# Kernel optimization log

Hardware: AMD Instinct MI355X
Metric: run time of the kernel (lower is better)

Reference implementation:

```python
import jax, jax.numpy as jnp
import numpy as np

B, T, D = 2, 2048, 1024
H, DK, DV, NH = 8, 128, 256, 2  # heads, key dim, value dim (expand_v=2), num_householder
CONV = 4
INTER = 2816
EPS = 1e-6


def rmsnorm(x, w):
    return x * jax.lax.rsqrt(jnp.mean(x * x, -1, keepdims=True) + EPS) * w


def l2norm(x):
    return x * jax.lax.rsqrt(jnp.sum(x * x, -1, keepdims=True) + 1e-6)


def causal_conv_silu(x, w):
    # depthwise causal conv1d with silu activation; x: [B,T,C], w: [C,K]
    K = w.shape[1]
    xp = jnp.pad(x, ((0, 0), (K - 1, 0), (0, 0)))
    y = sum(xp[:, i:i + x.shape[1], :] * w[:, i] for i in range(K))
    return jax.nn.silu(y)


def setup_inputs():
    key = jax.random.key(0)
    ks = jax.random.split(key, 16)
    s = 0.02
    return {
        "hidden_states": jax.random.normal(ks[0], (B, T, D), jnp.float32),
        "attn_norm_w": jnp.ones((D,), jnp.float32),
        "Wq": jax.random.normal(ks[1], (D, H * DK), jnp.float32) * s,
        "Wk": jax.random.normal(ks[2], (D, NH * H * DK), jnp.float32) * s,
        "Wv": jax.random.normal(ks[3], (D, NH * H * DV), jnp.float32) * s,
        "Wb": jax.random.normal(ks[4], (D, H * NH), jnp.float32) * s,
        "Wa": jax.random.normal(ks[5], (D, H), jnp.float32) * s,
        "A_log": jnp.log(jax.random.uniform(ks[6], (H,), jnp.float32, 1.0, 16.0)),
        "dt_bias": jax.random.normal(ks[7], (H,), jnp.float32) * 0.5,
        "conv_q_w": jax.random.normal(ks[8], (H * DK, CONV), jnp.float32) * 0.5,
        "conv_k_w": jax.random.normal(ks[9], (NH * H * DK, CONV), jnp.float32) * 0.5,
        "conv_v_w": jax.random.normal(ks[10], (NH * H * DV, CONV), jnp.float32) * 0.5,
        "Wg": jax.random.normal(ks[11], (D, H * DV), jnp.float32) * s,
        "o_norm_w": jnp.ones((DV,), jnp.float32),
        "Wo": jax.random.normal(ks[12], (H * DV, D), jnp.float32) * s,
        "mlp_norm_w": jnp.ones((D,), jnp.float32),
        "Wgate": jax.random.normal(ks[13], (D, 2 * INTER), jnp.float32) * s,
        "Wdown": jax.random.normal(ks[14], (INTER, D), jnp.float32) * s,
    }


def reference(hidden_states, attn_norm_w, Wq, Wk, Wv, Wb, Wa, A_log, dt_bias,
              conv_q_w, conv_k_w, conv_v_w, Wg, o_norm_w, Wo,
              mlp_norm_w, Wgate, Wdown):
    residual = hidden_states
    x = rmsnorm(hidden_states, attn_norm_w)

    # projections + short conv + silu, then L2-normalized q/k (gated delta rule)
    q = l2norm(causal_conv_silu(x @ Wq, conv_q_w).reshape(B, T, H, DK))
    k = l2norm(causal_conv_silu(x @ Wk, conv_k_w).reshape(B, T, NH, H, DK))
    v = causal_conv_silu(x @ Wv, conv_v_w).reshape(B, T, NH, H, DV)
    beta = jax.nn.sigmoid(x @ Wb).reshape(B, T, H, NH)
    g = -jnp.exp(A_log) * jax.nn.softplus(x @ Wa + dt_bias)  # [B,T,H] log-decay

    def step(S, inp):
        q_t, k_t, v_t, b_t, g_t = inp
        # forget gate applied once per token, then NH Householder delta-rule updates
        S = S * jnp.exp(g_t)[..., None, None]  # S: [B,H,DK,DV]
        for j in range(NH):
            kj, vj, bj = k_t[:, j], v_t[:, j], b_t[..., j]
            kS = jnp.einsum('bhk,bhkv->bhv', kj, S)
            S = S + bj[..., None, None] * jnp.einsum('bhk,bhv->bhkv', kj, vj - kS)
        o_t = jnp.einsum('bhk,bhkv->bhv', q_t, S)
        return S, o_t

    S0 = jnp.zeros((B, H, DK, DV), x.dtype)
    xs = (jnp.swapaxes(q, 0, 1), jnp.swapaxes(k, 0, 1), jnp.swapaxes(v, 0, 1),
          jnp.swapaxes(beta, 0, 1), jnp.swapaxes(g, 0, 1))
    _, o = jax.lax.scan(step, S0, xs)  # [T,B,H,DV]
    o = jnp.swapaxes(o, 0, 1)

    # gated RMSNorm output gate + output projection
    gate = (x @ Wg).reshape(B, T, H, DV)
    o = rmsnorm(o, o_norm_w) * jax.nn.silu(gate)
    hidden = residual + o.reshape(B, T, H * DV) @ Wo

    # GatedMLP (swiglu)
    y = rmsnorm(hidden, mlp_norm_w)
    gate_m, up = jnp.split(y @ Wgate, 2, -1)
    return hidden + (jax.nn.silu(gate_m) * up) @ Wdown
```

## Files before the change

kernel.cpp:

```cpp
#include <hip/hip_runtime.h>
#include <hip/hip_bf16.h>
#include <math.h>

#define Bq 2
#define Tq 2048
#define Dq 1024
#define Hq 8
#define DKq 128
#define DVq 256
#define NHq 2
#define BTq (Bq*Tq)
#define INTERq 2816

typedef __hip_bfloat16 bf16;
typedef short bfv8 __attribute__((ext_vector_type(8)));
typedef float f32v4 __attribute__((ext_vector_type(4)));

__device__ __forceinline__ float b2f(bf16 v){ return __bfloat162float(v); }
__device__ __forceinline__ bf16 f2b(float v){ return __float2bfloat16(v); }
__device__ __forceinline__ float bs2f(short s){
  union { short s; bf16 b; } u; u.s = s; return __bfloat162float(u.b);
}

__device__ __forceinline__ int is_f32(const unsigned* magic){ return magic[0] == 0x3F800000u; }

__device__ __forceinline__ float ldin(const void* p, int f32, size_t i){
  return f32 ? ((const float*)p)[i] : b2f(((const bf16*)p)[i]);
}

__device__ __forceinline__ void gload_lds16(const bf16* g, bf16* lds_uniform){
  __builtin_amdgcn_global_load_lds(
      (const __attribute__((address_space(1))) void*)g,
      (__attribute__((address_space(3))) void*)lds_uniform, 16, 0, 0);
}

__device__ __forceinline__ float wave_sum(float v){
  #pragma unroll
  for (int off = 32; off > 0; off >>= 1) v += __shfl_xor(v, off, 64);
  return v;
}

__device__ __forceinline__ float block_reduce_sum(float v, float* red){
  #pragma unroll
  for (int off = 32; off > 0; off >>= 1) v += __shfl_down(v, off, 64);
  int lane = threadIdx.x & 63, wid = threadIdx.x >> 6;
  if (lane == 0) red[wid] = v;
  __syncthreads();
  int nw = (blockDim.x + 63) >> 6;
  float tot = 0.f;
  for (int i = 0; i < nw; i++) tot += red[i];
  return tot;
}

struct WSplitArgs {
  const void* W[7];
  bf16* hi[7];
  bf16* lo[7];
  int K[7];
  int N[7];
  int il[7];
  int cum[8];
};

__global__ __launch_bounds__(256) void wsplit_all_kernel(WSplitArgs a,
    const unsigned* __restrict__ magic){
  __shared__ float tile[32][33];
  int f32 = is_f32(magic);
  int bid = blockIdx.x;
  int wi = 0;
  #pragma unroll
  for (int i = 1; i < 7; i++) if (bid >= a.cum[i]) wi = i;
  int rem = bid - a.cum[wi];
  const void* W = a.W[wi];
  bf16* hi = a.hi[wi];
  bf16* lo = a.lo[wi];
  int K = a.K[wi], N = a.N[wi], il = a.il[wi];
  int nbx = N >> 5;
  int n0 = (rem % nbx) * 32, k0 = (rem / nbx) * 32;
  int tx = threadIdx.x & 31, ty = threadIdx.x >> 5;
  #pragma unroll
  for (int r = 0; r < 4; r++){
    int kr = ty + r*8;
    tile[kr][tx] = ldin(W, f32, (size_t)(k0 + kr)*N + n0 + tx);
  }
  __syncthreads();
  int NH2 = N >> 1;
  #pragma unroll
  for (int r = 0; r < 4; r++){
    int nl = ty + r*8;
    int nr = n0 + nl;
    float v = tile[tx][nl];
    bf16 h = f2b(v);
    int cp = nr;
    if (il) cp = (nr < NH2) ? (((nr >> 4) << 5) | (nr & 15))
                            : ((((nr - NH2) >> 4) << 5) | 16 | ((nr - NH2) & 15));
    size_t idx = (size_t)cp*K + k0 + tx;
    hi[idx] = h;
    if (f32) lo[idx] = f2b(v - b2f(h));
  }
}

__device__ __forceinline__ void gemm_acc_bf16(const bf16* __restrict__ A,
    const bf16* __restrict__ Bh, int K, size_t bm, size_t bn,
    bf16* As, bf16* Bs, f32v4 (&acc)[4][4]){
  int tid = threadIdx.x;
  int lane = tid & 63, w = tid >> 6;
  int wm = w >> 1, wn = w & 1;
  int l15 = lane & 15, quad = lane >> 4;
  int srow = tid >> 2;
  int scol = (tid & 3) * 8;
  const bf16* Ag = A  + (bm + srow)*(size_t)K + scol;
  const bf16* Bg = Bh + (bn + srow)*(size_t)K + scol;
  int wslot = w * 512;
  int ntiles = K >> 5;
  int aoff = (wm*64 + l15)*32 + quad*8;
  int boff = (wn*64 + l15)*32 + quad*8;

#define STAGE(buf, kt) { \
    const bf16* a0 = Ag + ((size_t)(kt) << 5); \
    const bf16* b0 = Bg + ((size_t)(kt) << 5); \
    gload_lds16(a0,                &As[(buf)*4096 + wslot]); \
    gload_lds16(a0 + 64*(size_t)K, &As[(buf)*4096 + 2048 + wslot]); \
    gload_lds16(b0,                &Bs[(buf)*4096 + wslot]); \
    gload_lds16(b0 + 64*(size_t)K, &Bs[(buf)*4096 + 2048 + wslot]); }

  STAGE(0, 0)
  if (ntiles > 1) STAGE(1, 1)
  for (int t = 0; t < ntiles; ++t){
    if (t + 1 < ntiles) asm volatile("s_waitcnt vmcnt(4)" ::: "memory");
    else                asm volatile("s_waitcnt vmcnt(0)" ::: "memory");
    __builtin_amdgcn_sched_barrier(0);
    __builtin_amdgcn_s_barrier();
    __builtin_amdgcn_sched_barrier(0);
    int cur = t % 3;
    if (t + 2 < ntiles) STAGE((t + 2) % 3, t + 2)
    bfv8 a[4], bb[4];
    #pragma unroll
    for (int mt = 0; mt < 4; mt++)
      a[mt] = *(const bfv8*)(&As[cur*4096 + aoff + mt*16*32]);
    #pragma unroll
    for (int nn = 0; nn < 4; nn++)
      bb[nn] = *(const bfv8*)(&Bs[cur*4096 + boff + nn*16*32]);
    #pragma unroll
    for (int nn = 0; nn < 4; nn++)
      #pragma unroll
      for (int mt = 0; mt < 4; mt++)
        acc[mt][nn] = __builtin_amdgcn_mfma_f32_16x16x32_bf16(a[mt], bb[nn], acc[mt][nn], 0, 0, 0);
  }
#undef STAGE
}

__device__ __forceinline__ void gemm_acc_f32(const bf16* __restrict__ A,
    const bf16* __restrict__ Bh0, const bf16* __restrict__ Bl0,
    int K, size_t bm, size_t bn, f32v4 (&acc)[4][4]){
  int tid = threadIdx.x;
  int lane = tid & 63, w = tid >> 6;
  int wm = w >> 1, wn = w & 1;
  int l15 = lane & 15, quad = lane >> 4;
  const bf16* Ab = A   + (bm + wm*64 + l15)*(size_t)K + quad*8;
  const bf16* Bh = Bh0 + (bn + wn*64 + l15)*(size_t)K + quad*8;
  const bf16* Bl = Bl0 + (bn + wn*64 + l15)*(size_t)K + quad*8;
  for (int k0 = 0; k0 < K; k0 += 32){
    bfv8 a[4];
    #pragma unroll
    for (int mt = 0; mt < 4; mt++)
      a[mt] = *(const bfv8*)(Ab + (size_t)mt*16*K + k0);
    #pragma unroll
    for (int nt = 0; nt < 4; nt++){
      bfv8 bh = *(const bfv8*)(Bh + (size_t)nt*16*K + k0);
      bfv8 bl = *(const bfv8*)(Bl + (size_t)nt*16*K + k0);
      #pragma unroll
      for (int mt = 0; mt < 4; mt++){
        acc[mt][nt] = __builtin_amdgcn_mfma_f32_16x16x32_bf16(a[mt], bh, acc[mt][nt], 0, 0, 0);
        acc[mt][nt] = __builtin_amdgcn_mfma_f32_16x16x32_bf16(a[mt], bl, acc[mt][nt], 0, 0, 0);
      }
    }
  }
}

__global__ __launch_bounds__(256) void gemm_mfma_kernel(
    const bf16* __restrict__ A, const bf16* __restrict__ WThi, const bf16* __restrict__ WTlo,
    const unsigned* __restrict__ magic,
    const void* __restrict__ res, int res_mode,
    void* __restrict__ out, int out_mode,
    int M, int N, int K){
  __shared__ bf16 As[3*128*32];
  __shared__ bf16 Bs[3*128*32];
  int f32 = is_f32(magic);
  int tid = threadIdx.x;
  int lane = tid & 63, w = tid >> 6;
  int wm = w >> 1, wn = w & 1;
  int l15 = lane & 15, quad = lane >> 4;
  size_t bm = (size_t)blockIdx.x * 128, bn = (size_t)blockIdx.y * 128;

  f32v4 acc[4][4];
  #pragma unroll
  for (int mt = 0; mt < 4; mt++)
    #pragma unroll
    for (int nt = 0; nt < 4; nt++) acc[mt][nt] = 0.f;

  if (f32) gemm_acc_f32(A, WThi, WTlo, K, bm, bn, acc);
  else     gemm_acc_bf16(A, WThi, K, bm, bn, As, Bs, acc);

  if (out_mode == 3){
    #pragma unroll
    for (int mt = 0; mt < 4; mt++)
      #pragma unroll
      for (int nt = 0; nt < 4; nt += 2)
        #pragma unroll
        for (int r = 0; r < 4; r++){
          size_t row = bm + wm*64 + mt*16 + quad*4 + r;
          size_t col = (bn >> 1) + wn*32 + (nt >> 1)*16 + l15;
          float g = acc[mt][nt][r], u = acc[mt][nt+1][r];
          ((bf16*)out)[row*INTERq + col] = f2b(g / (1.f + __expf(-g)) * u);
        }
    return;
  }
  #pragma unroll
  for (int mt = 0; mt < 4; mt++)
    #pragma unroll
    for (int nt = 0; nt < 4; nt++)
      #pragma unroll
      for (int r = 0; r < 4; r++){
        size_t row = bm + wm*64 + mt*16 + quad*4 + r;
        size_t col = bn + wn*64 + nt*16 + l15;
        float v = acc[mt][nt][r];
        if (res_mode == 1) v += ldin(res, f32, row*N + col);
        else if (res_mode == 2) v += ((const float*)res)[row*N + col];
        if (out_mode == 0) ((float*)out)[row*N + col] = v;
        else if (out_mode == 1) ((bf16*)out)[row*N + col] = f2b(v);
        else { if (f32) ((float*)out)[row*N + col] = v; else ((bf16*)out)[row*N + col] = f2b(v); }
      }
}

struct QkvgArgs {
  const bf16* bh[4];
  const bf16* bl[4];
  bf16* out[4];
  int N[4];
  int yoff[5];
};

__global__ __launch_bounds__(256) void gemm_qkvg_kernel(
    const bf16* __restrict__ A, QkvgArgs a, const unsigned* __restrict__ magic){
  __shared__ bf16 As[3*128*32];
  __shared__ bf16 Bs[3*128*32];
  int f32 = is_f32(magic);
  int y = blockIdx.y;
  int g = 0;
  #pragma unroll
  for (int i = 1; i < 4; i++) if (y >= a.yoff[i]) g = i;
  size_t bm = (size_t)blockIdx.x * 128;
  size_t bn = (size_t)(y - a.yoff[g]) * 128;
  int N = a.N[g];

  f32v4 acc[4][4];
  #pragma unroll
  for (int mt = 0; mt < 4; mt++)
    #pragma unroll
    for (int nt = 0; nt < 4; nt++) acc[mt][nt] = 0.f;

  if (f32) gemm_acc_f32(A, a.bh[g], a.bl[g], 1024, bm, bn, acc);
  else     gemm_acc_bf16(A, a.bh[g], 1024, bm, bn, As, Bs, acc);

  bf16* out = a.out[g];
  int tid = threadIdx.x;
  int lane = tid & 63, w = tid >> 6;
  int wm = w >> 1, wn = w & 1;
  int l15 = lane & 15, quad = lane >> 4;
  #pragma unroll
  for (int mt = 0; mt < 4; mt++)
    #pragma unroll
    for (int nt = 0; nt < 4; nt++)
      #pragma unroll
      for (int r = 0; r < 4; r++){
        size_t row = bm + wm*64 + mt*16 + quad*4 + r;
        size_t col = bn + wn*64 + nt*16 + l15;
        out[row*N + col] = f2b(acc[mt][nt][r]);
      }
}

__global__ __launch_bounds__(256) void rmsnorm_betag_kernel(
    const void* __restrict__ hs, const void* __restrict__ attn_nw,
    const void* __restrict__ Wb, const void* __restrict__ Wa,
    const void* __restrict__ A_log, const void* __restrict__ dt_bias,
    const unsigned* __restrict__ magic,
    bf16* __restrict__ xout, float* __restrict__ beta, float* __restrict__ eg){
  __shared__ float xs[Dq];
  __shared__ float red[4];
  int f32 = is_f32(magic);
  size_t bt = blockIdx.x;
  int i0 = threadIdx.x * 4;
  float xv[4];
  if (f32){
    float4 v = *(const float4*)((const float*)hs + bt*Dq + i0);
    xv[0]=v.x; xv[1]=v.y; xv[2]=v.z; xv[3]=v.w;
  } else {
    short4 s = *(const short4*)((const bf16*)hs + bt*Dq + i0);
    xv[0]=bs2f(s.x); xv[1]=bs2f(s.y); xv[2]=bs2f(s.z); xv[3]=bs2f(s.w);
  }
  float ss = fmaf(xv[0],xv[0], fmaf(xv[1],xv[1], fmaf(xv[2],xv[2], xv[3]*xv[3])));
  float tot = block_reduce_sum(ss, red);
  float sc = rsqrtf(tot / (float)Dq + 1e-6f);
  bf16 ob[4];
  #pragma unroll
  for (int j = 0; j < 4; j++){
    float xn = xv[j] * sc * ldin(attn_nw, f32, i0 + j);
    ob[j] = f2b(xn);
    xs[i0 + j] = xn;
  }
  *(short4*)(xout + bt*Dq + i0) = *(short4*)ob;
  __syncthreads();

  int wv = threadIdx.x >> 6, lane = threadIdx.x & 63;
  #pragma unroll
  for (int r = 0; r < 6; r++){
    int n = wv*6 + r;
    float a = 0.f;
    if (n < 16){
      #pragma unroll
      for (int e = 0; e < 16; e++){
        int i = lane + 64*e;
        a = fmaf(xs[i], ldin(Wb, f32, (size_t)i*16 + n), a);
      }
    } else {
      int h = n - 16;
      #pragma unroll
      for (int e = 0; e < 16; e++){
        int i = lane + 64*e;
        a = fmaf(xs[i], ldin(Wa, f32, (size_t)i*8 + h), a);
      }
    }
    #pragma unroll
    for (int off = 32; off > 0; off >>= 1) a += __shfl_down(a, off, 64);
    if (lane == 0){
      if (n < 16){
        int h = n >> 1, j = n & 1;
        beta[(bt*Hq + h)*NHq + j] = 1.f / (1.f + expf(-a));
      } else {
        int h = n - 16;
        a += ldin(dt_bias, f32, h);
        float sp = (a > 20.f) ? a : log1pf(expf(a));
        eg[bt*Hq + h] = expf(-expf(ldin(A_log, f32, h)) * sp);
      }
    }
  }
}

__global__ __launch_bounds__(256) void rmsnorm_kernel(const void* __restrict__ in, int in_mode,
    const void* __restrict__ w, const unsigned* __restrict__ magic,
    bf16* __restrict__ out){
  __shared__ float red[4];
  int f32 = is_f32(magic);
  int inf32 = in_mode ? 1 : f32;
  size_t row = blockIdx.x;
  int i0 = threadIdx.x * 4;
  float xv[4];
  if (inf32){
    float4 v = *(const float4*)((const float*)in + row*Dq + i0);
    xv[0]=v.x; xv[1]=v.y; xv[2]=v.z; xv[3]=v.w;
  } else {
    short4 s = *(const short4*)((const bf16*)in + row*Dq + i0);
    xv[0]=bs2f(s.x); xv[1]=bs2f(s.y); xv[2]=bs2f(s.z); xv[3]=bs2f(s.w);
  }
  float ss = fmaf(xv[0],xv[0], fmaf(xv[1],xv[1], fmaf(xv[2],xv[2], xv[3]*xv[3])));
  float tot = block_reduce_sum(ss, red);
  float sc = rsqrtf(tot / (float)Dq + 1e-6f);
  bf16 ob[4];
  #pragma unroll
  for (int j = 0; j < 4; j++) ob[j] = f2b(xv[j] * sc * ldin(w, f32, i0 + j));
  *(short4*)(out + row*Dq + i0) = *(short4*)ob;
}

__global__ __launch_bounds__(64) void conv_qk_kernel(
    const bf16* __restrict__ qpre, const bf16* __restrict__ kpre,
    const void* __restrict__ wq, const void* __restrict__ wk,
    const unsigned* __restrict__ magic,
    float* __restrict__ qn, float* __restrict__ kn){
  int f32 = is_f32(magic);
  int bt = blockIdx.x;
  int t = bt & (Tq - 1);
  int yb = blockIdx.y;
  const bf16* in; const void* w; int C, cb; float* outf;
  if (yb < 8){ in = qpre; w = wq; C = 1024; cb = yb;     outf = qn; }
  else       { in = kpre; w = wk; C = 2048; cb = yb - 8; outf = kn; }
  int c = cb*128 + threadIdx.x*2;
  float a0 = 0.f, a1 = 0.f;
  #pragma unroll
  for (int i = 0; i < 4; i++){
    int tt = t - 3 + i;
    if (tt >= 0){
      short2 s = *(const short2*)(in + (size_t)(bt - 3 + i)*C + c);
      a0 = fmaf(bs2f(s.x), ldin(w, f32, (size_t)c*4 + i), a0);
      a1 = fmaf(bs2f(s.y), ldin(w, f32, (size_t)(c+1)*4 + i), a1);
    }
  }
  float y0 = a0 / (1.f + __expf(-a0));
  float y1 = a1 / (1.f + __expf(-a1));
  float tot = wave_sum(fmaf(y0, y0, y1*y1));
  float sc = rsqrtf(tot + 1e-6f);
  *(float2*)(outf + (size_t)bt*C + c) = make_float2(y0*sc, y1*sc);
}

__global__ __launch_bounds__(256) void conv_v_kernel(
    const bf16* __restrict__ in, const void* __restrict__ w,
    const unsigned* __restrict__ magic, bf16* __restrict__ out){
  int f32 = is_f32(magic);
  int bt = blockIdx.x;
  int t = bt & (Tq - 1);
  int c = blockIdx.y * 2048 + threadIdx.x * 8;
  float wv[32];
  #pragma unroll
  for (int j = 0; j < 8; j++)
    #pragma unroll
    for (int i = 0; i < 4; i++) wv[j*4+i] = ldin(w, f32, (size_t)(c+j)*4 + i);
  float acc[8] = {0,0,0,0,0,0,0,0};
  #pragma unroll
  for (int i = 0; i < 4; i++){
    int tt = t - 3 + i;
    if (tt >= 0){
      bfv8 v = *(const bfv8*)(in + (size_t)(bt - 3 + i)*4096 + c);
      #pragma unroll
      for (int j = 0; j < 8; j++) acc[j] = fmaf(bs2f(v[j]), wv[j*4+i], acc[j]);
    }
  }
  bf16 ob[8];
  #pragma unroll
  for (int j = 0; j < 8; j++) ob[j] = f2b(acc[j] / (1.f + __expf(-acc[j])));
  *(bfv8*)(out + (size_t)bt*4096 + c) = *(bfv8*)ob;
}

#define DPP_ADD(x, ctrl) ((x) + __int_as_float(__builtin_amdgcn_update_dpp( \
    0, __float_as_int(x), (ctrl), 0xF, 0xF, true)))
#define KRED(p) { p = DPP_ADD(p, 0x128); p = DPP_ADD(p, 0x124); \
                  p = DPP_ADD(p, 0x122); p = DPP_ADD(p, 0x121); }

__global__ __launch_bounds__(64, 1) void scan_kernel(
    const float* __restrict__ qn,
    const float* __restrict__ kn,
    const bf16*  __restrict__ vcv,
    const float* __restrict__ beta,
    const float* __restrict__ eg,
    float* __restrict__ o){
  int bh = blockIdx.x;
  int b = bh >> 3, h = bh & 7;
  int lane = threadIdx.x;
  int kg = lane & 15;
  int vloc = lane >> 4;
  int vv = blockIdx.y * 4 + vloc;
  int c0 = (h << 8) + vv;
  int c1 = 2048 + (h << 8) + vv;
  const size_t base = (size_t)b * Tq;
  const float* knh = kn + base*2048 + h*DKq + kg*8;
  const float* qnh = qn + (base*Hq + h)*(size_t)DKq + kg*8;
  const bf16*  vph = vcv + base*4096;
  const float* gh  = eg + base*Hq + h;
  const float2* bph = (const float2*)(beta + (base*Hq + h)*(size_t)NHq);
  float* oh = o + (base*Hq + h)*(size_t)DVq + vv;

  float4 S0 = {0,0,0,0}, S1 = {0,0,0,0};
#define SDOT(Ka, Kb, p) { \
    float e0 = fmaf(Ka.x, S0.x, Ka.y * S0.y); \
    float e1 = fmaf(Ka.z, S0.z, Ka.w * S0.w); \
    float e2 = fmaf(Kb.x, S1.x, Kb.y * S1.y); \
    float e3 = fmaf(Kb.z, S1.z, Kb.w * S1.w); \
    p = (e0 + e1) + (e2 + e3); }
#define SUPD(Ka, Kb, d) { \
    S0.x = fmaf(Ka.x, d, S0.x); S0.y = fmaf(Ka.y, d, S0.y); \
    S0.z = fmaf(Ka.z, d, S0.z); S0.w = fmaf(Ka.w, d, S0.w); \
    S1.x = fmaf(Kb.x, d, S1.x); S1.y = fmaf(Kb.y, d, S1.y); \
    S1.z = fmaf(Kb.z, d, S1.z); S1.w = fmaf(Kb.w, d, S1.w); }

  float4 A0E = *(const float4*)(knh);
  float4 A1E = *(const float4*)(knh + 4);
  float4 B0E = *(const float4*)(knh + 1024);
  float4 B1E = *(const float4*)(knh + 1028);
  float4 Q0E = *(const float4*)(qnh);
  float4 Q1E = *(const float4*)(qnh + 4);
  float4 A0O = *(const float4*)(knh + 2048);
  float4 A1O = *(const float4*)(knh + 2052);
  float4 B0O = *(const float4*)(knh + 3072);
  float4 B1O = *(const float4*)(knh + 3076);
  float4 Q0O = *(const float4*)(qnh + 1024);
  float4 Q1O = *(const float4*)(qnh + 1028);
  float  gE  = gh[0],   gO  = gh[8];
  float2 beE = bph[0],  beO = bph[8];
  float vaE = b2f(vph[c0]),        vbE = b2f(vph[c1]);
  float vaO = b2f(vph[4096 + c0]), vbO = b2f(vph[4096 + c1]);

#define STEP(A0,A1,B0,B1,Q0,Q1, gS, beS, vaS, vbS, t, tp) { \
    float egv = gS; \
    gS = gh[(tp)*8]; \
    S0.x *= egv; S0.y *= egv; S0.z *= egv; S0.w *= egv; \
    S1.x *= egv; S1.y *= egv; S1.z *= egv; S1.w *= egv; \
     \
    { float p; SDOT(A0, A1, p) \
      KRED(p) \
      float delta = beS.x * (vaS - p); \
      SUPD(A0, A1, delta) \
      A0 = *(const float4*)(knh + (tp)*2048); \
      A1 = *(const float4*)(knh + (tp)*2048 + 4); \
      vaS = b2f(vph[(tp)*4096 + c0]); } \
     \
    { float p; SDOT(B0, B1, p) \
      KRED(p) \
      float delta = beS.y * (vbS - p); \
      SUPD(B0, B1, delta) \
      B0 = *(const float4*)(knh + (tp)*2048 + 1024); \
      B1 = *(const float4*)(knh + (tp)*2048 + 1028); \
      vbS = b2f(vph[(tp)*4096 + c1]); } \
    beS = bph[(tp)*8]; \
     \
    { float p; SDOT(Q0, Q1, p) \
      KRED(p) \
      if ((lane & 15) == 0) oh[(t)*2048] = p; \
      Q0 = *(const float4*)(qnh + (tp)*1024); \
      Q1 = *(const float4*)(qnh + (tp)*1024 + 4); } \
    __builtin_amdgcn_sched_barrier(0); }

  for (int t = 0; t < Tq; t += 2){
    STEP(A0E,A1E,B0E,B1E,Q0E,Q1E, gE,beE,vaE,vbE, t,   t+2)
    STEP(A0O,A1O,B0O,B1O,Q0O,Q1O, gO,beO,vaO,vbO, t+1, t+3)
  }
#undef STEP
#undef SDOT
#undef SUPD
}

__global__ __launch_bounds__(64) void gate_o_kernel(
    const float* __restrict__ o, const void* __restrict__ onw,
    const unsigned* __restrict__ magic,
    const bf16* __restrict__ gate, bf16* __restrict__ og){
  int f32 = is_f32(magic);
  size_t bth = blockIdx.x;
  int d0 = threadIdx.x * 4;
  float4 v = *(const float4*)(o + bth*DVq + d0);
  float tot = wave_sum(fmaf(v.x,v.x, fmaf(v.y,v.y, fmaf(v.z,v.z, v.w*v.w))));
  float sc = rsqrtf(tot / (float)DVq + 1e-6f);
  short4 gs = *(const short4*)(gate + bth*DVq + d0);
  float gv[4] = {bs2f(gs.x), bs2f(gs.y), bs2f(gs.z), bs2f(gs.w)};
  float vv[4] = {v.x, v.y, v.z, v.w};
  bf16 ob[4];
  #pragma unroll
  for (int j = 0; j < 4; j++){
    float silu = gv[j] / (1.f + __expf(-gv[j]));
    ob[j] = f2b(vv[j] * sc * ldin(onw, f32, d0 + j) * silu);
  }
  *(short4*)(og + bth*DVq + d0) = *(short4*)ob;
}

extern "C" void kernel_launch(void* const* d_in, const int* in_sizes, int n_in,
                              void* d_out, int out_size, void* d_ws, size_t ws_size,
                              hipStream_t stream){
  const void* hs      = d_in[0];
  const unsigned* magic = (const unsigned*)d_in[1];
  const void* attn_nw = d_in[1];
  const void* Wq      = d_in[2];
  const void* Wk      = d_in[3];
  const void* Wv      = d_in[4];
  const void* Wb      = d_in[5];
  const void* Wa      = d_in[6];
  const void* A_log   = d_in[7];
  const void* dt_bias = d_in[8];
  const void* conv_q  = d_in[9];
  const void* conv_k  = d_in[10];
  const void* conv_v  = d_in[11];
  const void* Wg      = d_in[12];
  const void* o_nw    = d_in[13];
  const void* Wo      = d_in[14];
  const void* mlp_nw  = d_in[15];
  const void* Wgate   = d_in[16];
  const void* Wdown   = d_in[17];

  char* ws = (char*)d_ws;
  const size_t MB = (size_t)1 << 20;
  size_t X     = 0;
  size_t QPRE  = 8*MB;
  size_t KPRE  = 16*MB;
  size_t VPRE  = 32*MB;
  size_t GATE  = 64*MB;
  size_t QN    = 80*MB;
  size_t KN    = 96*MB;
  size_t HID   = 128*MB;
  size_t BETA  = 144*MB;
  size_t Gb    = 144*MB + 512*1024;
  size_t VCV    = 0;
  size_t O      = 32*MB;
  size_t OG     = QN;
  size_t Y      = KN;
  size_t MID    = O;
  size_t W0 = 145*MB;
  size_t WTQh = W0 +  0*MB, WTQl = W0 +  2*MB;
  size_t WTKh = W0 +  4*MB, WTKl = W0 +  8*MB;
  size_t WTVh = W0 + 12*MB, WTVl = W0 + 20*MB;
  size_t WTGh = W0 + 28*MB, WTGl = W0 + 32*MB;
  size_t WTOh = W0 + 36*MB, WTOl = W0 + 40*MB;
  size_t WTUh = W0 + 44*MB, WTUl = W0 + 56*MB;
  size_t WTDh = W0 + 68*MB, WTDl = W0 + 74*MB;
  (void)ws_size; (void)in_sizes; (void)n_in; (void)out_size;

  WSplitArgs wa;
  {
    const void* Ws[7]  = {Wq, Wk, Wv, Wg, Wo, Wgate, Wdown};
    size_t hio[7]      = {WTQh, WTKh, WTVh, WTGh, WTOh, WTUh, WTDh};
    size_t loo[7]      = {WTQl, WTKl, WTVl, WTGl, WTOl, WTUl, WTDl};
    int Ks[7]          = {1024, 1024, 1024, 1024, 2048, 1024, 2816};
    int Ns[7]          = {1024, 2048, 4096, 2048, 1024, 5632, 1024};
    int ils[7]         = {0, 0, 0, 0, 0, 1, 0};
    int cums[8]        = {0, 1024, 3072, 7168, 9216, 11264, 16896, 19712};
    for (int i = 0; i < 7; i++){
      wa.W[i] = Ws[i]; wa.hi[i] = (bf16*)(ws + hio[i]); wa.lo[i] = (bf16*)(ws + loo[i]);
      wa.K[i] = Ks[i]; wa.N[i] = Ns[i]; wa.il[i] = ils[i]; wa.cum[i] = cums[i];
    }
    wa.cum[7] = cums[7];
    wsplit_all_kernel<<<19712, 256, 0, stream>>>(wa, magic);
  }

  rmsnorm_betag_kernel<<<BTq, 256, 0, stream>>>(hs, attn_nw, Wb, Wa, A_log, dt_bias,
      magic, (bf16*)(ws+X), (float*)(ws+BETA), (float*)(ws+Gb));

  QkvgArgs qa;
  {
    size_t bho[4] = {WTQh, WTKh, WTVh, WTGh};
    size_t blo[4] = {WTQl, WTKl, WTVl, WTGl};
    size_t oo[4]  = {QPRE, KPRE, VPRE, GATE};
    int Ns[4]     = {1024, 2048, 4096, 2048};
    int yo[5]     = {0, 8, 24, 56, 72};
    for (int i = 0; i < 4; i++){
      qa.bh[i] = (const bf16*)(ws + bho[i]); qa.bl[i] = (const bf16*)(ws + blo[i]);
      qa.out[i] = (bf16*)(ws + oo[i]); qa.N[i] = Ns[i]; qa.yoff[i] = yo[i];
    }
    qa.yoff[4] = yo[4];
    gemm_qkvg_kernel<<<dim3(32, 72), 256, 0, stream>>>((const bf16*)(ws+X), qa, magic);
  }

  conv_qk_kernel<<<dim3(BTq, 24), 64, 0, stream>>>((const bf16*)(ws+QPRE), (const bf16*)(ws+KPRE),
      conv_q, conv_k, magic, (float*)(ws+QN), (float*)(ws+KN));
  conv_v_kernel<<<dim3(BTq, 2), 256, 0, stream>>>((const bf16*)(ws+VPRE), conv_v, magic, (bf16*)(ws+VCV));

  scan_kernel<<<dim3(Bq*Hq, DVq/4), 64, 0, stream>>>(
      (const float*)(ws+QN), (const float*)(ws+KN), (const bf16*)(ws+VCV),
      (const float*)(ws+BETA), (const float*)(ws+Gb), (float*)(ws+O));

  gate_o_kernel<<<BTq*Hq, 64, 0, stream>>>((const float*)(ws+O), o_nw, magic,
      (const bf16*)(ws+GATE), (bf16*)(ws+OG));

  gemm_mfma_kernel<<<dim3(32, 8), 256, 0, stream>>>((bf16*)(ws+OG), (bf16*)(ws+WTOh), (bf16*)(ws+WTOl),
      magic, hs, 1, ws+HID, 0, BTq, 1024, 2048);

  rmsnorm_kernel<<<BTq, 256, 0, stream>>>(ws+HID, 1, mlp_nw, magic, (bf16*)(ws+Y));

  gemm_mfma_kernel<<<dim3(32, 44), 256, 0, stream>>>((bf16*)(ws+Y), (bf16*)(ws+WTUh), (bf16*)(ws+WTUl),
      magic, nullptr, 0, ws+MID, 3, BTq, 5632, 1024);

  gemm_mfma_kernel<<<dim3(32, 8), 256, 0, stream>>>((bf16*)(ws+MID), (bf16*)(ws+WTDh), (bf16*)(ws+WTDl),
      magic, ws+HID, 2, d_out, 2, BTq, 1024, 2816);
}
```

Measured before the change: 2.353 ms.

## Process two value-column groups per wave in scan kernel to raise ILP

Each scan wave now carries two independent state slices, at value columns vv and vv+128, and shares the k, q, beta and gate loads between them. The grid's y dimension is halved to match. The aim is to hide the serial DPP-reduction latency of the recurrence with a second independent chain and to cut redundant key/query loads. In exchange each wave uses more registers and does twice the work, and half as many waves are resident across the CUs.

```diff
diff --git a/kernel.cpp b/kernel.cpp
--- a/kernel.cpp
+++ b/kernel.cpp
@@ -448,8 +448,10 @@
   int kg = lane & 15;
   int vloc = lane >> 4;
   int vv = blockIdx.y * 4 + vloc;
-  int c0 = (h << 8) + vv;
-  int c1 = 2048 + (h << 8) + vv;
+  int c0a = (h << 8) + vv;
+  int c1a = 2048 + (h << 8) + vv;
+  int c0b = c0a + 128;
+  int c1b = c1a + 128;
   const size_t base = (size_t)b * Tq;
   const float* knh = kn + base*2048 + h*DKq + kg*8;
   const float* qnh = qn + (base*Hq + h)*(size_t)DKq + kg*8;
@@ -458,14 +460,15 @@
   const float2* bph = (const float2*)(beta + (base*Hq + h)*(size_t)NHq);
   float* oh = o + (base*Hq + h)*(size_t)DVq + vv;
 
-  float4 S0 = {0,0,0,0}, S1 = {0,0,0,0};
-#define SDOT(Ka, Kb, p) { \
+  float4 S0a = {0,0,0,0}, S1a = {0,0,0,0};
+  float4 S0b = {0,0,0,0}, S1b = {0,0,0,0};
+#define SDOT(Ka, Kb, S0, S1, p) { \
     float e0 = fmaf(Ka.x, S0.x, Ka.y * S0.y); \
     float e1 = fmaf(Ka.z, S0.z, Ka.w * S0.w); \
     float e2 = fmaf(Kb.x, S1.x, Kb.y * S1.y); \
     float e3 = fmaf(Kb.z, S1.z, Kb.w * S1.w); \
     p = (e0 + e1) + (e2 + e3); }
-#define SUPD(Ka, Kb, d) { \
+#define SUPD(Ka, Kb, S0, S1, d) { \
     S0.x = fmaf(Ka.x, d, S0.x); S0.y = fmaf(Ka.y, d, S0.y); \
     S0.z = fmaf(Ka.z, d, S0.z); S0.w = fmaf(Ka.w, d, S0.w); \
     S1.x = fmaf(Kb.x, d, S1.x); S1.y = fmaf(Kb.y, d, S1.y); \
@@ -485,42 +488,58 @@
   float4 Q1O = *(const float4*)(qnh + 1028);
   float  gE  = gh[0],   gO  = gh[8];
   float2 beE = bph[0],  beO = bph[8];
-  float vaE = b2f(vph[c0]),        vbE = b2f(vph[c1]);
-  float vaO = b2f(vph[4096 + c0]), vbO = b2f(vph[4096 + c1]);
-
-#define STEP(A0,A1,B0,B1,Q0,Q1, gS, beS, vaS, vbS, t, tp) { \
+  float vaEa = b2f(vph[c0a]),        vbEa = b2f(vph[c1a]);
+  float vaEb = b2f(vph[c0b]),        vbEb = b2f(vph[c1b]);
+  float vaOa = b2f(vph[4096 + c0a]), vbOa = b2f(vph[4096 + c1a]);
+  float vaOb = b2f(vph[4096 + c0b]), vbOb = b2f(vph[4096 + c1b]);
+
+#define STEP(A0,A1,B0,B1,Q0,Q1, gS, beS, vaA, vbA, vaB, vbB, t, tp) { \
     float egv = gS; \
     gS = gh[(tp)*8]; \
-    S0.x *= egv; S0.y *= egv; S0.z *= egv; S0.w *= egv; \
-    S1.x *= egv; S1.y *= egv; S1.z *= egv; S1.w *= egv; \
+    S0a.x *= egv; S0a.y *= egv; S0a.z *= egv; S0a.w *= egv; \
+    S1a.x *= egv; S1a.y *= egv; S1a.z *= egv; S1a.w *= egv; \
+    S0b.x *= egv; S0b.y *= egv; S0b.z *= egv; S0b.w *= egv; \
+    S1b.x *= egv; S1b.y *= egv; S1b.z *= egv; S1b.w *= egv; \
      \
-    { float p; SDOT(A0, A1, p) \
-      KRED(p) \
-      float delta = beS.x * (vaS - p); \
-      SUPD(A0, A1, delta) \
+    { float pa, pb; \
+      SDOT(A0, A1, S0a, S1a, pa) \
+      SDOT(A0, A1, S0b, S1b, pb) \
+      KRED(pa) KRED(pb) \
+      float da = beS.x * (vaA - pa); \
+      float db = beS.x * (vaB - pb); \
+      SUPD(A0, A1, S0a, S1a, da) \
+      SUPD(A0, A1, S0b, S1b, db) \
       A0 = *(const float4*)(knh + (tp)*2048); \
       A1 = *(const float4*)(knh + (tp)*2048 + 4); \
-      vaS = b2f(vph[(tp)*4096 + c0]); } \
+      vaA = b2f(vph[(tp)*4096 + c0a]); \
+      vaB = b2f(vph[(tp)*4096 + c0b]); } \
      \
-    { float p; SDOT(B0, B1, p) \
-      KRED(p) \
-      float delta = beS.y * (vbS - p); \
-      SUPD(B0, B1, delta) \
+    { float pa, pb; \
+      SDOT(B0, B1, S0a, S1a, pa) \
+      SDOT(B0, B1, S0b, S1b, pb) \
+      KRED(pa) KRED(pb) \
+      float da = beS.y * (vbA - pa); \
+      float db = beS.y * (vbB - pb); \
+      SUPD(B0, B1, S0a, S1a, da) \
+      SUPD(B0, B1, S0b, S1b, db) \
       B0 = *(const float4*)(knh + (tp)*2048 + 1024); \
       B1 = *(const float4*)(knh + (tp)*2048 + 1028); \
-      vbS = b2f(vph[(tp)*4096 + c1]); } \
+      vbA = b2f(vph[(tp)*4096 + c1a]); \
+      vbB = b2f(vph[(tp)*4096 + c1b]); } \
     beS = bph[(tp)*8]; \
      \
-    { float p; SDOT(Q0, Q1, p) \
-      KRED(p) \
-      if ((lane & 15) == 0) oh[(t)*2048] = p; \
+    { float pa, pb; \
+      SDOT(Q0, Q1, S0a, S1a, pa) \
+      SDOT(Q0, Q1, S0b, S1b, pb) \
+      KRED(pa) KRED(pb) \
+      if ((lane & 15) == 0){ oh[(t)*2048] = pa; oh[(t)*2048 + 128] = pb; } \
       Q0 = *(const float4*)(qnh + (tp)*1024); \
       Q1 = *(const float4*)(qnh + (tp)*1024 + 4); } \
     __builtin_amdgcn_sched_barrier(0); }
 
   for (int t = 0; t < Tq; t += 2){
-    STEP(A0E,A1E,B0E,B1E,Q0E,Q1E, gE,beE,vaE,vbE, t,   t+2)
-    STEP(A0O,A1O,B0O,B1O,Q0O,Q1O, gO,beO,vaO,vbO, t+1, t+3)
+    STEP(A0E,A1E,B0E,B1E,Q0E,Q1E, gE,beE, vaEa,vbEa,vaEb,vbEb, t,   t+2)
+    STEP(A0O,A1O,B0O,B1O,Q0O,Q1O, gO,beO, vaOa,vbOa,vaOb,vbOb, t+1, t+3)
   }
 #undef STEP
 #undef SDOT
@@ -638,7 +657,7 @@
       conv_q, conv_k, magic, (float*)(ws+QN), (float*)(ws+KN));
   conv_v_kernel<<<dim3(BTq, 2), 256, 0, stream>>>((const bf16*)(ws+VPRE), conv_v, magic, (bf16*)(ws+VCV));
 
-  scan_kernel<<<dim3(Bq*Hq, DVq/4), 64, 0, stream>>>(
+  scan_kernel<<<dim3(Bq*Hq, DVq/8), 64, 0, stream>>>(
       (const float*)(ws+QN), (const float*)(ws+KN), (const bf16*)(ws+VCV),
       (const float*)(ws+BETA), (const float*)(ws+Gb), (float*)(ws+O));
 
```

Result: slower. 2.486 ms (+5.7%).
